# Performance work log

Measured on AMD Instinct MI355X. Metric: run time of the kernel, lower is better.

The kernel has to match this reference:

```python
import jax, jax.numpy as jnp
import numpy as np

N, S, F, O, MAXM = 8192, 8192, 64, 64, 10
K0, K1, K2, K3 = 0.5, 0.05, -0.05, 0.05


def setup_inputs() -> dict:
    key = jax.random.key(0)
    kx, kp, kn, km, ks, kw, kb = jax.random.split(key, 7)
    x = jax.random.normal(kx, (N, F), dtype=jnp.float32)
    lap_p = jax.random.normal(kp, (N, N), dtype=jnp.float32)
    lap_n = jax.random.normal(kn, (N, N), dtype=jnp.float32)
    # Build incidence matrix [N, S]: each structure (column) has 3, 4, or 10 member nodes.
    members = jax.random.randint(km, (S, MAXM), 0, N)              # [S, 10]
    sizes = jnp.array([3, 4, 10])[jax.random.randint(ks, (S,), 0, 3)]  # [S]
    valid = (jnp.arange(MAXM)[None, :] < sizes[:, None]).astype(jnp.float32)  # [S, 10]
    rows = members.reshape(-1)
    cols = jnp.repeat(jnp.arange(S), MAXM)
    inc = jnp.zeros((N, S), jnp.float32).at[rows, cols].max(valid.reshape(-1))
    stdv = 1.0 / np.sqrt(O)
    weight = jax.random.uniform(kw, (F, O), jnp.float32, -stdv, stdv)
    bias = jax.random.uniform(kb, (O,), jnp.float32, -stdv, stdv)
    return {"input": x, "lap_matrix_p": lap_p, "lap_matrix_n": lap_n,
            "incidence_matrix_preoder": inc, "weight": weight, "bias": bias}


def reference(input, lap_matrix_p, lap_matrix_n, incidence_matrix_preoder, weight, bias):
    x = input
    inc = incidence_matrix_preoder  # [N, S], 0/1
    # Laplacian sin-diffusion term
    out1 = K0 * x + K1 * jnp.sin(lap_matrix_p @ x) + K2 * jnp.sin(lap_matrix_n @ x)
    # Per-structure term. For a structure with members {i0 < i1 < ... < i_{m-1}}:
    #   t = tanh((m-1)*x[i0] - sum_{j>0} x[ij]) = tanh(m*x[i0] - sum_all_members)
    size = jnp.sum(inc, axis=0)                       # [S]
    first = jnp.argmax(inc, axis=0)                   # [S], smallest member index (first 1)
    sum_members = inc.T @ x                           # [S, F]
    t = jnp.tanh(size[:, None] * x[first] - sum_members)  # [S, F]
    valid = ((size == 3) | (size == 4) | (size == 10)).astype(x.dtype)  # only these sizes count
    out2 = K3 * (inc @ (t * valid[:, None]))          # scatter back to member nodes
    out = out1 + out2
    return out @ weight + bias
```

## Files before the change

### kernel.cpp

```cpp
#include <hip/hip_runtime.h>
#include <cstdint>
#include <cstddef>

#define NN 8192
#define SS 8192
#define FF 64
#define MAXM 10

typedef __attribute__((ext_vector_type(8))) short bf16x8;
typedef __attribute__((ext_vector_type(4))) float f32x4;

__device__ __forceinline__ void splitf(float a, unsigned short& h, unsigned short& l) {
    unsigned u = __float_as_uint(a);
    unsigned hb = u & 0xffff0000u;
    h = (unsigned short)(hb >> 16);
    float r = a - __uint_as_float(hb);
    l = (unsigned short)(__float_as_uint(r) >> 16);
}

__global__ __launch_bounds__(256) void k_prep(const float* __restrict__ x,
                                              unsigned short* __restrict__ xh,
                                              unsigned short* __restrict__ xl) {
    __shared__ float tile[64][65];
    int b = blockIdx.x;
    int tr = threadIdx.x >> 6;
    int tc = threadIdx.x & 63;
#pragma unroll
    for (int rr = 0; rr < 16; ++rr) {
        int row = rr * 4 + tr;
        tile[row][tc] = x[(size_t)(b * 64 + row) * 64 + tc];
    }
    __syncthreads();
#pragma unroll
    for (int rr = 0; rr < 16; ++rr) {
        int c = rr * 4 + tr;
        int k = tc;
        float a = tile[k][c];
        unsigned short h, l;
        splitf(a, h, l);
        xh[(size_t)c * NN + b * 64 + k] = h;
        xl[(size_t)c * NN + b * 64 + k] = l;
    }
}

#define KCH   512
#define NSTEP 16

__device__ __forceinline__ void loadA(const float* __restrict__ ap0,
                                      const float* __restrict__ ap1,
                                      int ko, f32x4 av[2][2]) {
    av[0][0] = *(const f32x4*)(ap0 + ko);
    av[0][1] = *(const f32x4*)(ap0 + ko + 4);
    av[1][0] = *(const f32x4*)(ap1 + ko);
    av[1][1] = *(const f32x4*)(ap1 + ko + 4);
}

__device__ __forceinline__ void loadB(const unsigned short* __restrict__ bh0,
                                      const unsigned short* __restrict__ bl0,
                                      int ko, bf16x8 bh[4], bf16x8 bl[4]) {
#pragma unroll
    for (int n = 0; n < 4; ++n) {
        bh[n] = *(const bf16x8*)(bh0 + (size_t)n * (16 * NN) + ko);
        bl[n] = *(const bf16x8*)(bl0 + (size_t)n * (16 * NN) + ko);
    }
}

__device__ __forceinline__ void gstep(const f32x4 av[2][2],
                                      const bf16x8 bh[4], const bf16x8 bl[4],
                                      f32x4 c[2][4]) {
#pragma unroll
    for (int t = 0; t < 2; ++t) {
        bf16x8 ah, al;
#pragma unroll
        for (int jj = 0; jj < 8; ++jj) {
            float a = av[t][jj >> 2][jj & 3];
            unsigned u = __float_as_uint(a);
            unsigned hb = u & 0xffff0000u;
            float r = a - __uint_as_float(hb);
            ah[jj] = (short)(hb >> 16);
            al[jj] = (short)(__float_as_uint(r) >> 16);
        }
#pragma unroll
        for (int n = 0; n < 4; ++n) {
            c[t][n] = __builtin_amdgcn_mfma_f32_16x16x32_bf16(ah, bh[n], c[t][n], 0, 0, 0);
            c[t][n] = __builtin_amdgcn_mfma_f32_16x16x32_bf16(ah, bl[n], c[t][n], 0, 0, 0);
            c[t][n] = __builtin_amdgcn_mfma_f32_16x16x32_bf16(al, bh[n], c[t][n], 0, 0, 0);
        }
    }
}

__global__ __launch_bounds__(256, 4) void k_gemm(const float* __restrict__ Lp,
                                                 const float* __restrict__ Ln,
                                                 const unsigned short* __restrict__ xh,
                                                 const unsigned short* __restrict__ xl,
                                                 float* __restrict__ accP,
                                                 float* __restrict__ accN) {
    const int wave = threadIdx.x >> 6;
    const int lane = threadIdx.x & 63;
    const int l16 = lane & 15;
    const int l4 = lane >> 4;
    const float* A = blockIdx.z ? Ln : Lp;
    float* acc = blockIdx.z ? accN : accP;
    const int row0 = blockIdx.x * 128 + wave * 32;
    const int k0 = blockIdx.y * KCH;

    const float* ap0 = A + (size_t)(row0 + l16) * NN + k0 + l4 * 8;
    const float* ap1 = ap0 + (size_t)16 * NN;
    const unsigned short* bh0 = xh + (size_t)l16 * NN + k0 + l4 * 8;
    const unsigned short* bl0 = xl + (size_t)l16 * NN + k0 + l4 * 8;

    f32x4 c[2][4] = {};
    f32x4 avA[2][2], avB[2][2];
    bf16x8 bh[4], bl[4];

    loadA(ap0, ap1, 0, avA);
    for (int s = 0; s < NSTEP; s += 2) {
        loadB(bh0, bl0, s * 32, bh, bl);
        loadA(ap0, ap1, (s + 1) * 32, avB);
        gstep(avA, bh, bl, c);
        loadB(bh0, bl0, (s + 1) * 32, bh, bl);
        if (s + 2 < NSTEP) loadA(ap0, ap1, (s + 2) * 32, avA);
        gstep(avB, bh, bl, c);
    }

#pragma unroll
    for (int t = 0; t < 2; ++t)
#pragma unroll
        for (int n = 0; n < 4; ++n)
#pragma unroll
            for (int r = 0; r < 4; ++r) {
                int row = row0 + t * 16 + l4 * 4 + r;
                int col = n * 16 + l16;
                atomicAdd(&acc[(size_t)row * FF + col], c[t][n][r]);
            }
}

__global__ __launch_bounds__(256) void k_scan(const float4* __restrict__ inc4,
                                              int* __restrict__ cnt,
                                              int* __restrict__ firstA,
                                              int* __restrict__ members) {
    size_t b = (size_t)blockIdx.x * 1024 + threadIdx.x;
    float4 v0 = inc4[b];
    float4 v1 = inc4[b + 256];
    float4 v2 = inc4[b + 512];
    float4 v3 = inc4[b + 768];
#pragma unroll
    for (int k = 0; k < 4; ++k) {
        float4 v = (k == 0) ? v0 : (k == 1) ? v1 : (k == 2) ? v2 : v3;
        size_t base = (b + (size_t)k * 256) * 4;
        int i = (int)(base >> 13);
        int j = (int)(base & (SS - 1));
        float vv[4] = {v.x, v.y, v.z, v.w};
#pragma unroll
        for (int c = 0; c < 4; ++c) {
            if (vv[c] != 0.0f) {
                int slot = atomicAdd(&cnt[j + c], 1);
                if (slot < MAXM) members[(j + c) * MAXM + slot] = i;
                atomicMin(&firstA[j + c], i);
            }
        }
    }
}

__global__ __launch_bounds__(256) void k_struct(const float* __restrict__ x,
                                                const int* __restrict__ cnt,
                                                const int* __restrict__ firstA,
                                                const int* __restrict__ members,
                                                float* __restrict__ out2) {
    int j = blockIdx.x * 4 + (threadIdx.x >> 6);
    int f = threadIdx.x & 63;
    int m = cnt[j];
    if (!(m == 3 || m == 4 || m == 10)) return;
    int fi = firstA[j];
    float xf = x[(size_t)fi * FF + f];
    float s = 0.0f;
    int mem[MAXM];
#pragma unroll
    for (int t = 0; t < MAXM; ++t)
        if (t < m) { mem[t] = members[j * MAXM + t]; s += x[(size_t)mem[t] * FF + f]; }
    float tv = tanhf((float)m * xf - s);
    float val = 0.05f * tv;
#pragma unroll
    for (int t = 0; t < MAXM; ++t)
        if (t < m) atomicAdd(&out2[(size_t)mem[t] * FF + f], val);
}

__global__ __launch_bounds__(256) void k_final(const float* __restrict__ x,
                                               const float* __restrict__ accP,
                                               const float* __restrict__ accN,
                                               const float* __restrict__ out2,
                                               const float* __restrict__ W,
                                               const float* __restrict__ bias,
                                               float* __restrict__ out) {
    __shared__ float Wl[64 * 64];
    __shared__ float vbuf[4][64];
    int tid = threadIdx.x;
#pragma unroll
    for (int i = tid; i < 4096; i += 256) Wl[i] = W[i];
    int r = tid >> 6, f = tid & 63;
    size_t row = (size_t)blockIdx.x * 4 + r;
    size_t idx = row * FF + f;
    float v = 0.5f * x[idx] + 0.05f * sinf(accP[idx]) - 0.05f * sinf(accN[idx]) + out2[idx];
    vbuf[r][f] = v;
    __syncthreads();
    float o = bias[f];
#pragma unroll
    for (int k = 0; k < 64; ++k) o += vbuf[r][k] * Wl[k * 64 + f];
    out[idx] = o;
}

extern "C" void kernel_launch(void* const* d_in, const int* in_sizes, int n_in,
                              void* d_out, int out_size, void* d_ws, size_t ws_size,
                              hipStream_t stream) {
    const float* x    = (const float*)d_in[0];
    const float* Lp   = (const float*)d_in[1];
    const float* Ln   = (const float*)d_in[2];
    const float* inc  = (const float*)d_in[3];
    const float* W    = (const float*)d_in[4];
    const float* bias = (const float*)d_in[5];
    float* out = (float*)d_out;

    char* ws = (char*)d_ws;
    float* accP = (float*)(ws);
    float* accN = (float*)(ws + (2u << 20));
    float* out2 = (float*)(ws + (4u << 20));
    int* cnt    = (int*)(ws + (6u << 20));
    int* firstA = (int*)(ws + (6u << 20) + 32768);
    int* members= (int*)(ws + (6u << 20) + 65536);
    unsigned short* xhv = (unsigned short*)(ws + (6u << 20) + 65536 + 327680);
    unsigned short* xlv = xhv + (size_t)NN * FF;

    hipMemsetAsync(ws, 0, (6u << 20) + 32768, stream);
    hipMemsetAsync(firstA, 0x7f, 32768, stream);

    k_prep<<<128, 256, 0, stream>>>(x, xhv, xlv);
    k_gemm<<<dim3(64, 16, 2), 256, 0, stream>>>(Lp, Ln, xhv, xlv, accP, accN);
    k_scan<<<16384, 256, 0, stream>>>((const float4*)inc, cnt, firstA, members);
    k_struct<<<2048, 256, 0, stream>>>(x, cnt, firstA, members, out2);
    k_final<<<2048, 256, 0, stream>>>(x, accP, accN, out2, W, bias, out);
}
```

Baseline: 774.0 us.

## Stage Laplacian A tiles through LDS with async global_load_lds double buffering

The GEMM kernel now streams fp32 Laplacian rows into a double-buffered, XOR-swizzled shared-memory tile using direct global-to-LDS loads, instead of having each lane load its A fragment straight into registers. Manual vmcnt/lgkmcnt waits pipeline the next stage's loads and the B fragment loads against the MFMA compute of the current stage. The aim is more coalesced A reads (each row read as full contiguous 128-byte segments) and better latency hiding. It adds 32KB of LDS per block, which may limit occupancy, and the hand-counted waitcnt values must match the actual number of outstanding loads to stay correct.

```diff
diff --git a/kernel.cpp b/kernel.cpp
--- a/kernel.cpp
+++ b/kernel.cpp
@@ -46,28 +46,9 @@
 #define KCH   512
 #define NSTEP 16
 
-__device__ __forceinline__ void loadA(const float* __restrict__ ap0,
-                                      const float* __restrict__ ap1,
-                                      int ko, f32x4 av[2][2]) {
-    av[0][0] = *(const f32x4*)(ap0 + ko);
-    av[0][1] = *(const f32x4*)(ap0 + ko + 4);
-    av[1][0] = *(const f32x4*)(ap1 + ko);
-    av[1][1] = *(const f32x4*)(ap1 + ko + 4);
-}
-
-__device__ __forceinline__ void loadB(const unsigned short* __restrict__ bh0,
-                                      const unsigned short* __restrict__ bl0,
-                                      int ko, bf16x8 bh[4], bf16x8 bl[4]) {
-#pragma unroll
-    for (int n = 0; n < 4; ++n) {
-        bh[n] = *(const bf16x8*)(bh0 + (size_t)n * (16 * NN) + ko);
-        bl[n] = *(const bf16x8*)(bl0 + (size_t)n * (16 * NN) + ko);
-    }
-}
-
-__device__ __forceinline__ void gstep(const f32x4 av[2][2],
-                                      const bf16x8 bh[4], const bf16x8 bl[4],
-                                      f32x4 c[2][4]) {
+__device__ __forceinline__ void gcompute(const f32x4 av[2][2],
+                                         const bf16x8 bh[4], const bf16x8 bl[4],
+                                         f32x4 c[2][4]) {
 #pragma unroll
     for (int t = 0; t < 2; ++t) {
         bf16x8 ah, al;
@@ -95,6 +76,7 @@
                                                  const unsigned short* __restrict__ xl,
                                                  float* __restrict__ accP,
                                                  float* __restrict__ accN) {
+    __shared__ float lds[2][4][32][32];
     const int wave = threadIdx.x >> 6;
     const int lane = threadIdx.x & 63;
     const int l16 = lane & 15;
@@ -104,24 +86,81 @@
     const int row0 = blockIdx.x * 128 + wave * 32;
     const int k0 = blockIdx.y * KCH;
 
-    const float* ap0 = A + (size_t)(row0 + l16) * NN + k0 + l4 * 8;
-    const float* ap1 = ap0 + (size_t)16 * NN;
+    const int srow = lane >> 3;
+    const int sslot = (lane & 7) ^ srow;
+    const float* gA = A + (size_t)(row0 + srow) * NN + k0 + sslot * 4;
+
     const unsigned short* bh0 = xh + (size_t)l16 * NN + k0 + l4 * 8;
     const unsigned short* bl0 = xl + (size_t)l16 * NN + k0 + l4 * 8;
 
+    const int rs0 = ((l4 * 2 + 0) ^ (l16 & 7)) * 4;
+    const int rs1 = ((l4 * 2 + 1) ^ (l16 & 7)) * 4;
+
+#define STAGE(BUF, KS) do {                                                     \
+    const float* _s = gA + (KS) * 32;                                           \
+    _Pragma("unroll")                                                           \
+    for (int q = 0; q < 4; ++q)                                                 \
+        __builtin_amdgcn_global_load_lds(                                       \
+            (const __attribute__((address_space(1))) void*)(_s + (size_t)q * 8 * NN), \
+            (__attribute__((address_space(3))) void*)&lds[BUF][wave][8 * q][0], \
+            16, 0, 0);                                                          \
+} while (0)
+
+#define LOADB(FH, FL, KS) do {                                                  \
+    _Pragma("unroll")                                                           \
+    for (int n = 0; n < 4; ++n) {                                               \
+        FH[n] = *(const bf16x8*)(bh0 + (size_t)n * (16 * NN) + (KS) * 32);      \
+        FL[n] = *(const bf16x8*)(bl0 + (size_t)n * (16 * NN) + (KS) * 32);      \
+    }                                                                           \
+} while (0)
+
+#define READAV(BUF) do {                                                        \
+    av[0][0] = *(const f32x4*)&lds[BUF][wave][l16][rs0];                        \
+    av[0][1] = *(const f32x4*)&lds[BUF][wave][l16][rs1];                        \
+    av[1][0] = *(const f32x4*)&lds[BUF][wave][16 + l16][rs0];                   \
+    av[1][1] = *(const f32x4*)&lds[BUF][wave][16 + l16][rs1];                   \
+} while (0)
+
+#define WAITVM12() asm volatile("s_waitcnt vmcnt(12)" ::: "memory")
+#define WAITVM8()  asm volatile("s_waitcnt vmcnt(8)" ::: "memory")
+#define WAITLGKM() asm volatile("s_waitcnt lgkmcnt(0)" ::: "memory")
+
     f32x4 c[2][4] = {};
-    f32x4 avA[2][2], avB[2][2];
-    bf16x8 bh[4], bl[4];
-
-    loadA(ap0, ap1, 0, avA);
-    for (int s = 0; s < NSTEP; s += 2) {
-        loadB(bh0, bl0, s * 32, bh, bl);
-        loadA(ap0, ap1, (s + 1) * 32, avB);
-        gstep(avA, bh, bl, c);
-        loadB(bh0, bl0, (s + 1) * 32, bh, bl);
-        if (s + 2 < NSTEP) loadA(ap0, ap1, (s + 2) * 32, avA);
-        gstep(avB, bh, bl, c);
-    }
+    f32x4 av[2][2];
+    bf16x8 b0h[4], b0l[4], b1h[4], b1l[4];
+
+    STAGE(0, 0);
+    LOADB(b0h, b0l, 0);
+    STAGE(1, 1);
+
+    for (int s = 0; s < NSTEP - 2; s += 2) {
+        WAITVM12();
+        READAV(0);
+        WAITLGKM();
+        STAGE(0, s + 2);
+        LOADB(b1h, b1l, s + 1);
+        gcompute(av, b0h, b0l, c);
+        WAITVM12();
+        READAV(1);
+        WAITLGKM();
+        STAGE(1, s + 3);
+        LOADB(b0h, b0l, s + 2);
+        gcompute(av, b1h, b1l, c);
+    }
+    WAITVM12();
+    READAV(0);
+    LOADB(b1h, b1l, NSTEP - 1);
+    gcompute(av, b0h, b0l, c);
+    WAITVM8();
+    READAV(1);
+    gcompute(av, b1h, b1l, c);
+
+#undef STAGE
+#undef LOADB
+#undef READAV
+#undef WAITVM12
+#undef WAITVM8
+#undef WAITLGKM
 
 #pragma unroll
     for (int t = 0; t < 2; ++t)
```

After: 780.0 us. No clear change (+0.8%).
